# Kernel optimization log

Measured on AMD Instinct MI355X. Metric: run time of the kernel, lower is better.

The kernel has to match this reference:

```python
import jax, jax.numpy as jnp
import numpy as np

B, L, D_MODEL, H, D_K, D_V, C = 4, 2048, 512, 8, 64, 64, 5
LN_EPS = 1e-5


def setup_inputs() -> dict:
    key = jax.random.key(0)
    ks = jax.random.split(key, 9)
    u_k = min(int(C * np.log(L)), L)  # 38
    s = 1.0 / np.sqrt(D_MODEL)
    return {
        "input_Q": jax.random.normal(ks[0], (B, L, D_MODEL), jnp.float32),
        "input_K": jax.random.normal(ks[1], (B, L, D_MODEL), jnp.float32),
        "input_V": jax.random.normal(ks[2], (B, L, D_MODEL), jnp.float32),
        "W_Q": jax.random.normal(ks[3], (D_MODEL, H * D_K), jnp.float32) * s,
        "W_K": jax.random.normal(ks[4], (D_MODEL, H * D_K), jnp.float32) * s,
        "W_V": jax.random.normal(ks[5], (D_MODEL, H * D_V), jnp.float32) * s,
        "W_fc": jax.random.normal(ks[6], (H * D_V, D_MODEL), jnp.float32) * (1.0 / np.sqrt(H * D_V)),
        "ln_gamma": jnp.ones((D_MODEL,), jnp.float32),
        "ln_beta": jnp.zeros((D_MODEL,), jnp.float32),
        "index_sample": jax.random.randint(ks[7], (L, u_k), 0, L, jnp.int32),
    }


def reference(input_Q, input_K, input_V, W_Q, W_K, W_V, W_fc, ln_gamma, ln_beta, index_sample):
    Bb, L_Q, _ = input_Q.shape
    L_K = input_K.shape[1]
    u_q = min(int(C * np.log(L_Q)), L_Q)  # n_top queries kept

    # projections -> (B, H, L, d)
    Q = (input_Q @ W_Q).reshape(Bb, L_Q, H, D_K).transpose(0, 2, 1, 3)
    K = (input_K @ W_K).reshape(Bb, L_K, H, D_K).transpose(0, 2, 1, 3)
    V = (input_V @ W_V).reshape(Bb, L_K, H, D_V).transpose(0, 2, 1, 3)

    # sampled QK scores: gather u_k random keys per query position
    K_sample = K[:, :, index_sample, :]                      # (B,H,L_Q,u_k,d_k)
    QK_sample = jnp.einsum('bhqe,bhqke->bhqk', Q, K_sample)  # (B,H,L_Q,u_k)

    # sparsity measure M = max - mean, top-u_q queries
    M = QK_sample.max(axis=-1) - QK_sample.mean(axis=-1)     # (B,H,L_Q)
    _, idx = jax.lax.top_k(M, u_q)                           # (B,H,u_q)

    # attention only for selected queries
    Q_sel = jnp.take_along_axis(Q, idx[..., None], axis=2)   # (B,H,u_q,d_k)
    scores = jnp.einsum('bhue,bhke->bhuk', Q_sel, K) / np.sqrt(D_K)
    attn = jax.nn.softmax(scores, axis=-1)
    values = jnp.einsum('bhuk,bhkd->bhud', attn, V)          # (B,H,u_q,d_v)

    # initial context = mean of V (attn_mask is None), scatter selected rows
    context = jnp.broadcast_to(V.mean(axis=2, keepdims=True), (Bb, H, L_Q, D_V))
    bb = jnp.arange(Bb)[:, None, None]
    hh = jnp.arange(H)[None, :, None]
    context = context.at[bb, hh, idx].set(values)

    context = context.transpose(0, 2, 1, 3).reshape(Bb, L_Q, H * D_V)
    out = context @ W_fc                                     # dropout p=0.0

    y = out + input_Q
    mu = y.mean(axis=-1, keepdims=True)
    var = jnp.mean(jnp.square(y - mu), axis=-1, keepdims=True)
    y = (y - mu) / jnp.sqrt(var + LN_EPS) * ln_gamma + ln_beta
    return y, idx
```

## Files before the change

kernel.cpp:

```cpp
#include <hip/hip_runtime.h>
#include <hip/hip_bf16.h>

#define NB 4
#define NL 2048
#define NH 8
#define NDM 512
#define ND 64
#define KSPLIT 16
#define KTILE 32
#define QB 8

typedef __attribute__((ext_vector_type(8))) short short8b;
typedef __attribute__((ext_vector_type(4))) float f32x4;

__global__ void wconv(const float* __restrict__ W, unsigned short* __restrict__ WT) {
  const int g = blockIdx.x * 256 + threadIdx.x;
  const int k = g >> 9, c = g & 511;
  __hip_bfloat16 hb = __float2bfloat16(W[(size_t)k * 512 + c]);
  WT[(size_t)c * 512 + k] = *reinterpret_cast<unsigned short*>(&hb);
}

__global__ void vmean_colmean(const float* __restrict__ inV, float* __restrict__ parts) {
  const int b = blockIdx.x, seg = blockIdx.y, t = threadIdx.x;
  const float* p = inV + ((size_t)b * NL + seg * 32) * NDM;
  float s0 = 0.f, s1 = 0.f;
  for (int r = 0; r < 32; ++r) {
    s0 += p[(size_t)r * NDM + t];
    s1 += p[(size_t)r * NDM + 256 + t];
  }
  parts[((size_t)b * 64 + seg) * NDM + t] = s0;
  parts[((size_t)b * 64 + seg) * NDM + 256 + t] = s1;
}
__global__ void vmean_gemm(const float* __restrict__ parts, const float* __restrict__ Wv,
                           float* __restrict__ Vm) {
  __shared__ float cm[512];
  const int b = blockIdx.x, t = threadIdx.x;
  float a0 = 0.f, a1 = 0.f;
  for (int g = 0; g < 64; ++g) {
    a0 += parts[((size_t)b * 64 + g) * NDM + t];
    a1 += parts[((size_t)b * 64 + g) * NDM + 256 + t];
  }
  cm[t] = a0 * (1.f / 2048.f);
  cm[t + 256] = a1 * (1.f / 2048.f);
  __syncthreads();
  const int c0 = blockIdx.y * 256 + t;
  float acc = 0.f;
  for (int k = 0; k < 512; ++k) acc += cm[k] * Wv[(size_t)k * NDM + c0];
  Vm[b * 512 + c0] = acc;
}

__global__ __launch_bounds__(256, 4) void proj3(
    const float* __restrict__ AQ, const float* __restrict__ AK,
    const float* __restrict__ wQm, const float* __restrict__ wKm,
    int gh0, float* __restrict__ Qc, float* __restrict__ Kc) {
  __shared__ float As_[32 * 132];
  __shared__ float Ws_[32 * 68];
  const int tid = threadIdx.x;
  const int bm = blockIdx.x;
  const int hl = blockIdx.y;
  const int mat = blockIdx.z;
  const int bh = gh0 + hl;
  const int b = bh >> 3, h = bh & 7;
  const float* A = (mat == 0) ? AQ : AK;
  const float* W = (mat == 0) ? wQm : wKm;
  float* D = (mat == 0) ? Qc : Kc;
  const float* Ab = A + (size_t)b * NL * NDM;
  const int colbase = h * 64;
  const int tm = tid >> 4, tn = tid & 15;
  float acc[8][4] = {};
  for (int k0 = 0; k0 < 512; k0 += 32) {
#pragma unroll
    for (int i = 0; i < 4; ++i) {
      int s = tid + i * 256;
      int r = s >> 3, c4 = (s & 7) * 4;
      float4 v = *reinterpret_cast<const float4*>(Ab + (size_t)(bm * 128 + r) * 512 + k0 + c4);
      As_[(c4 + 0) * 132 + r] = v.x;
      As_[(c4 + 1) * 132 + r] = v.y;
      As_[(c4 + 2) * 132 + r] = v.z;
      As_[(c4 + 3) * 132 + r] = v.w;
    }
#pragma unroll
    for (int i = 0; i < 2; ++i) {
      int s = tid + i * 256;
      int r = s >> 4, c4 = (s & 15) * 4;
      *reinterpret_cast<float4*>(&Ws_[r * 68 + c4]) =
          *reinterpret_cast<const float4*>(W + (size_t)(k0 + r) * 512 + colbase + c4);
    }
    __syncthreads();
#pragma unroll
    for (int kk = 0; kk < 32; ++kk) {
      float4 a0 = *reinterpret_cast<const float4*>(&As_[kk * 132 + tm * 4]);
      float4 a1 = *reinterpret_cast<const float4*>(&As_[kk * 132 + 64 + tm * 4]);
      float4 w  = *reinterpret_cast<const float4*>(&Ws_[kk * 68 + tn * 4]);
      float a[8] = {a0.x, a0.y, a0.z, a0.w, a1.x, a1.y, a1.z, a1.w};
      float wv[4] = {w.x, w.y, w.z, w.w};
#pragma unroll
      for (int ii = 0; ii < 8; ++ii)
#pragma unroll
        for (int jj = 0; jj < 4; ++jj) acc[ii][jj] += a[ii] * wv[jj];
    }
    __syncthreads();
  }
#pragma unroll
  for (int ii = 0; ii < 8; ++ii) {
    int row = bm * 128 + ((ii < 4) ? (tm * 4 + ii) : (64 + tm * 4 + (ii - 4)));
    float4 v = make_float4(acc[ii][0], acc[ii][1], acc[ii][2], acc[ii][3]);
    *reinterpret_cast<float4*>(D + ((size_t)hl * NL + row) * ND + tn * 4) = v;
  }
}

__global__ __launch_bounds__(256) void projV_mfma(
    const float* __restrict__ AV, const unsigned short* __restrict__ WT,
    int gh0, float* __restrict__ Vc) {
  const int wv = threadIdx.x >> 6, l = threadIdx.x & 63;
  const int bm = blockIdx.x;
  const int hl = blockIdx.y;
  const int bh = gh0 + hl;
  const int b = bh >> 3, h = bh & 7;
  const float* Ab = AV + (size_t)b * NL * NDM;
  const int row = bm * 64 + wv * 16 + (l & 15);
  const int kg = (l >> 4) * 8;
  f32x4 acc0 = {}, acc1 = {}, acc2 = {}, acc3 = {};
  for (int k0 = 0; k0 < 512; k0 += 32) {
    const float* ap = Ab + (size_t)row * 512 + k0 + kg;
    float4 v0 = *reinterpret_cast<const float4*>(ap);
    float4 v1 = *reinterpret_cast<const float4*>(ap + 4);
    short8b af;
    {
      __hip_bfloat16 hb;
      hb = __float2bfloat16(v0.x); af[0] = *reinterpret_cast<short*>(&hb);
      hb = __float2bfloat16(v0.y); af[1] = *reinterpret_cast<short*>(&hb);
      hb = __float2bfloat16(v0.z); af[2] = *reinterpret_cast<short*>(&hb);
      hb = __float2bfloat16(v0.w); af[3] = *reinterpret_cast<short*>(&hb);
      hb = __float2bfloat16(v1.x); af[4] = *reinterpret_cast<short*>(&hb);
      hb = __float2bfloat16(v1.y); af[5] = *reinterpret_cast<short*>(&hb);
      hb = __float2bfloat16(v1.z); af[6] = *reinterpret_cast<short*>(&hb);
      hb = __float2bfloat16(v1.w); af[7] = *reinterpret_cast<short*>(&hb);
    }
    const unsigned short* wp = WT + (size_t)(h * 64 + (l & 15)) * 512 + k0 + kg;
    short8b b0 = *reinterpret_cast<const short8b*>(wp);
    short8b b1 = *reinterpret_cast<const short8b*>(wp + 16 * 512);
    short8b b2 = *reinterpret_cast<const short8b*>(wp + 32 * 512);
    short8b b3 = *reinterpret_cast<const short8b*>(wp + 48 * 512);
    acc0 = __builtin_amdgcn_mfma_f32_16x16x32_bf16(af, b0, acc0, 0, 0, 0);
    acc1 = __builtin_amdgcn_mfma_f32_16x16x32_bf16(af, b1, acc1, 0, 0, 0);
    acc2 = __builtin_amdgcn_mfma_f32_16x16x32_bf16(af, b2, acc2, 0, 0, 0);
    acc3 = __builtin_amdgcn_mfma_f32_16x16x32_bf16(af, b3, acc3, 0, 0, 0);
  }
  const int rbase = bm * 64 + wv * 16 + (l >> 4) * 4;
  const int col = l & 15;
#pragma unroll
  for (int j = 0; j < 4; ++j) {
    size_t o = ((size_t)hl * NL + rbase + j) * ND + col;
    Vc[o] = acc0[j];
    Vc[o + 16] = acc1[j];
    Vc[o + 32] = acc2[j];
    Vc[o + 48] = acc3[j];
  }
}

template <int UK>
__global__ __launch_bounds__(256) void sampleV_fused(
    const float* __restrict__ Q, const float* __restrict__ K,
    const int* __restrict__ sampP, float* __restrict__ M,
    const float* __restrict__ AV, const unsigned short* __restrict__ WT,
    int gh0, float* __restrict__ Vc, int nsampBlk) {
  if ((int)blockIdx.x >= nsampBlk) {
    const int vblk = blockIdx.x - nsampBlk;
    const int bm = vblk & 31;
    const int hl = vblk >> 5;
    const int wv = threadIdx.x >> 6, l = threadIdx.x & 63;
    const int bh = gh0 + hl;
    const int b = bh >> 3, h = bh & 7;
    const float* Ab = AV + (size_t)b * NL * NDM;
    const int row = bm * 64 + wv * 16 + (l & 15);
    const int kg = (l >> 4) * 8;
    f32x4 acc0 = {}, acc1 = {}, acc2 = {}, acc3 = {};
    for (int k0 = 0; k0 < 512; k0 += 32) {
      const float* ap = Ab + (size_t)row * 512 + k0 + kg;
      float4 v0 = *reinterpret_cast<const float4*>(ap);
      float4 v1 = *reinterpret_cast<const float4*>(ap + 4);
      short8b af;
      {
        __hip_bfloat16 hb;
        hb = __float2bfloat16(v0.x); af[0] = *reinterpret_cast<short*>(&hb);
        hb = __float2bfloat16(v0.y); af[1] = *reinterpret_cast<short*>(&hb);
        hb = __float2bfloat16(v0.z); af[2] = *reinterpret_cast<short*>(&hb);
        hb = __float2bfloat16(v0.w); af[3] = *reinterpret_cast<short*>(&hb);
        hb = __float2bfloat16(v1.x); af[4] = *reinterpret_cast<short*>(&hb);
        hb = __float2bfloat16(v1.y); af[5] = *reinterpret_cast<short*>(&hb);
        hb = __float2bfloat16(v1.z); af[6] = *reinterpret_cast<short*>(&hb);
        hb = __float2bfloat16(v1.w); af[7] = *reinterpret_cast<short*>(&hb);
      }
      const unsigned short* wp = WT + (size_t)(h * 64 + (l & 15)) * 512 + k0 + kg;
      short8b b0 = *reinterpret_cast<const short8b*>(wp);
      short8b b1 = *reinterpret_cast<const short8b*>(wp + 16 * 512);
      short8b b2 = *reinterpret_cast<const short8b*>(wp + 32 * 512);
      short8b b3 = *reinterpret_cast<const short8b*>(wp + 48 * 512);
      acc0 = __builtin_amdgcn_mfma_f32_16x16x32_bf16(af, b0, acc0, 0, 0, 0);
      acc1 = __builtin_amdgcn_mfma_f32_16x16x32_bf16(af, b1, acc1, 0, 0, 0);
      acc2 = __builtin_amdgcn_mfma_f32_16x16x32_bf16(af, b2, acc2, 0, 0, 0);
      acc3 = __builtin_amdgcn_mfma_f32_16x16x32_bf16(af, b3, acc3, 0, 0, 0);
    }
    const int rbase = bm * 64 + wv * 16 + (l >> 4) * 4;
    const int col = l & 15;
#pragma unroll
    for (int j = 0; j < 4; ++j) {
      size_t o = ((size_t)hl * NL + rbase + j) * ND + col;
      Vc[o] = acc0[j];
      Vc[o + 16] = acc1[j];
      Vc[o + 32] = acc2[j];
      Vc[o + 48] = acc3[j];
    }
    return;
  }
  __shared__ float KsAll[4][UK * 66];
  __shared__ float QsAll[4][68];
  const int wv = threadIdx.x >> 6, l = threadIdx.x & 63;
  const int gq = blockIdx.x * 4 + wv;
  const int hl = gq >> 11;
  const int q = gq & 2047;
  float* Ks = KsAll[wv];
  float* Qs = QsAll[wv];
  const float* Kb = K + (size_t)hl * NL * ND;
  Qs[l] = Q[(size_t)gq * ND + l];
  const int base = __builtin_amdgcn_readfirstlane(q) * UK;
#pragma unroll
  for (int r = 0; r < UK; ++r) {
    int kk = sampP[base + r] & (NL - 1);
    Ks[r * 66 + l] = Kb[(size_t)kk * ND + l];
  }
  __syncthreads();
  const int myk = (l < UK) ? l : (UK - 1);
  float acc = 0.f;
#pragma unroll
  for (int j = 0; j < 32; ++j) {
    float2 kv = *reinterpret_cast<const float2*>(&Ks[myk * 66 + 2 * j]);
    float2 qv = *reinterpret_cast<const float2*>(&Qs[2 * j]);
    acc += kv.x * qv.x + kv.y * qv.y;
  }
  float mval = (l < UK) ? acc : -1e30f;
  float sval = (l < UK) ? acc : 0.f;
#pragma unroll
  for (int o = 32; o; o >>= 1) {
    mval = fmaxf(mval, __shfl_xor(mval, o, 64));
    sval += __shfl_xor(sval, o, 64);
  }
  if (l == 0) M[gq] = mval - sval * (1.f / (float)UK);
}

__global__ void sample_scores_gen(const float* __restrict__ Q, const float* __restrict__ K,
                                  const int* __restrict__ sampP, float* __restrict__ M, int uk) {
  const int wave = threadIdx.x >> 6, lane = threadIdx.x & 63;
  const int gq = blockIdx.x * 4 + wave;
  const int hl = gq >> 11;
  const int q = gq & 2047;
  const float qv = Q[(size_t)gq * ND + lane];
  const float* Kbase = K + (size_t)hl * NL * ND;
  float mx = -1e30f, sm = 0.f;
  for (int k = 0; k < uk; ++k) {
    int kidx = sampP[q * uk + k] & (NL - 1);
    float p = qv * Kbase[(size_t)kidx * ND + lane];
#pragma unroll
    for (int o = 32; o; o >>= 1) p += __shfl_xor(p, o, 64);
    mx = fmaxf(mx, p);
    sm += p;
  }
  if (lane == 0) M[gq] = mx - sm / (float)uk;
}

__global__ void topk_kernel(const float* __restrict__ M, int* __restrict__ idxo,
                            float* __restrict__ outIdx, short* __restrict__ selmap,
                            int gh0, int uq) {
  __shared__ float mv[2048];
  __shared__ float bwv[4];
  __shared__ int bwi[4];
  const int bh = blockIdx.x, t = threadIdx.x;
  const int bhg = gh0 + bh;
  const int bb = bhg >> 3, hh = bhg & 7;
  float lv = -1e38f; int li = 1 << 30;
#pragma unroll
  for (int i = 0; i < 8; ++i) {
    int id = t + i * 256;
    float v = M[(size_t)bh * 2048 + id];
    mv[id] = v;
    if (v > lv || (v == lv && id < li)) { lv = v; li = id; }
  }
  __syncthreads();
  for (int it = 0; it < uq; ++it) {
    float bv = lv; int bi = li;
#pragma unroll
    for (int o = 32; o; o >>= 1) {
      float ov = __shfl_xor(bv, o, 64);
      int oi = __shfl_xor(bi, o, 64);
      if (ov > bv || (ov == bv && oi < bi)) { bv = ov; bi = oi; }
    }
    if ((t & 63) == 0) { bwv[t >> 6] = bv; bwi[t >> 6] = bi; }
    __syncthreads();
    float gb = bwv[0]; int gi = bwi[0];
#pragma unroll
    for (int w = 1; w < 4; ++w) {
      if (bwv[w] > gb || (bwv[w] == gb && bwi[w] < gi)) { gb = bwv[w]; gi = bwi[w]; }
    }
    const int sel = gi & (NL - 1);
    if (t == 0) {
      idxo[bh * uq + it] = sel;
      outIdx[bh * uq + it] = (float)sel;
      selmap[((size_t)bb * NL + sel) * NH + hh] = (short)it;
    }
    if ((sel & 255) == t) {
      mv[sel] = -1e38f;
      lv = -1e38f; li = 1 << 30;
#pragma unroll
      for (int i = 0; i < 8; ++i) {
        int id = t + i * 256;
        float v = mv[id];
        if (v > lv || (v == lv && id < li)) { lv = v; li = id; }
      }
    }
    __syncthreads();
  }
}

__global__ __launch_bounds__(256) void attn_part(
    const float* __restrict__ Qw, const float* __restrict__ Kw, const float* __restrict__ Vw,
    const int* __restrict__ idxo, float* __restrict__ pacc, float* __restrict__ pml, int uq) {
  __shared__ float Qs[QB][68];
  __shared__ float Ks[KTILE][68];
  __shared__ float Vs[KTILE][68];
  __shared__ float sc[QB][34];
  const int hl = blockIdx.x, qg = blockIdx.y, ks = blockIdx.z;
  const int t = threadIdx.x;
#pragma unroll
  for (int i = 0; i < 2; ++i) {
    int s = t + i * 256;
    int q = s >> 6, d = s & 63;
    int u = qg * QB + q;
    float v = 0.f;
    if (u < uq) {
      int qi = idxo[hl * uq + u] & (NL - 1);
      v = Qw[((size_t)hl * NL + qi) * ND + d];
    }
    Qs[q][d] = v;
  }
  float m_run = -1e30f, l_run = 0.f;
  float a0 = 0.f, a1 = 0.f;
  const int q2 = t >> 5, ln = t & 31;
  __syncthreads();
  const int kbeg = ks * (NL / KSPLIT);
  for (int k0 = kbeg; k0 < kbeg + NL / KSPLIT; k0 += KTILE) {
#pragma unroll
    for (int i = 0; i < 2; ++i) {
      int s = t + i * 256;
      int r = s >> 4, c4 = (s & 15) * 4;
      *reinterpret_cast<float4*>(&Ks[r][c4]) =
          *reinterpret_cast<const float4*>(Kw + ((size_t)hl * NL + k0 + r) * ND + c4);
      *reinterpret_cast<float4*>(&Vs[r][c4]) =
          *reinterpret_cast<const float4*>(Vw + ((size_t)hl * NL + k0 + r) * ND + c4);
    }
    __syncthreads();
    {
      const int q = t & 7, kk = t >> 3;
      float d0 = 0.f;
#pragma unroll
      for (int dd = 0; dd < 64; dd += 4) {
        float4 qv = *reinterpret_cast<const float4*>(&Qs[q][dd]);
        float4 ka = *reinterpret_cast<const float4*>(&Ks[kk][dd]);
        d0 += qv.x * ka.x + qv.y * ka.y + qv.z * ka.z + qv.w * ka.w;
      }
      sc[q][kk] = d0 * 0.125f;
    }
    __syncthreads();
    {
      float s0 = sc[q2][ln];
      float tmax = s0;
#pragma unroll
      for (int o = 16; o; o >>= 1) tmax = fmaxf(tmax, __shfl_xor(tmax, o, 64));
      float mnew = fmaxf(m_run, tmax);
      float scl = __expf(m_run - mnew);
      float p0 = __expf(s0 - mnew);
      float tsum = p0;
#pragma unroll
      for (int o = 16; o; o >>= 1) tsum += __shfl_xor(tsum, o, 64);
      l_run = l_run * scl + tsum;
      m_run = mnew;
      sc[q2][ln] = p0;
      a0 *= scl; a1 *= scl;
#pragma unroll 8
      for (int k = 0; k < KTILE; ++k) {
        float p = sc[q2][k];
        a0 += p * Vs[k][2 * ln];
        a1 += p * Vs[k][2 * ln + 1];
      }
    }
    __syncthreads();
  }
  const int u = qg * QB + q2;
  if (u < uq) {
    size_t g = ((size_t)hl * uq + u) * KSPLIT + ks;
    pacc[g * ND + 2 * ln] = a0;
    pacc[g * ND + 2 * ln + 1] = a1;
    if (ln == 0) { pml[g * 2] = m_run; pml[g * 2 + 1] = l_run; }
  }
}

__global__ void corr_merge(const float* __restrict__ pacc, const float* __restrict__ pml,
                           const float* __restrict__ Vm, const float* __restrict__ Wfc,
                           float* __restrict__ corr, int uq) {
  __shared__ float diff[64];
  const int g = blockIdx.x, t = threadIdx.x;
  const int bh = g / uq;
  const int h = bh & 7;
  if (t < 64) {
    float mstar = -1e30f;
#pragma unroll
    for (int s = 0; s < KSPLIT; ++s) mstar = fmaxf(mstar, pml[((size_t)g * KSPLIT + s) * 2]);
    float num = 0.f, den = 0.f;
#pragma unroll
    for (int s = 0; s < KSPLIT; ++s) {
      float e = __expf(pml[((size_t)g * KSPLIT + s) * 2] - mstar);
      den += e * pml[((size_t)g * KSPLIT + s) * 2 + 1];
      num += e * pacc[((size_t)g * KSPLIT + s) * ND + t];
    }
    diff[t] = num / den - Vm[(size_t)bh * 64 + t];
  }
  __syncthreads();
  float a0 = 0.f, a1 = 0.f;
#pragma unroll
  for (int d = 0; d < 64; ++d) {
    a0 += diff[d] * Wfc[(size_t)(h * 64 + d) * 512 + t];
    a1 += diff[d] * Wfc[(size_t)(h * 64 + d) * 512 + t + 256];
  }
  corr[(size_t)g * 512 + t] = a0;
  corr[(size_t)g * 512 + t + 256] = a1;
}

__global__ void base_gemm(const float* __restrict__ Vm, const float* __restrict__ Wfc,
                          float* __restrict__ base) {
  __shared__ float vm[512];
  const int b = blockIdx.x, t = threadIdx.x;
  vm[t] = Vm[b * 512 + t];
  vm[t + 256] = Vm[b * 512 + t + 256];
  __syncthreads();
  const int c0 = blockIdx.y * 256 + t;
  float acc = 0.f;
  for (int k = 0; k < 512; ++k) acc += vm[k] * Wfc[(size_t)k * 512 + c0];
  base[b * 512 + c0] = acc;
}

__global__ void ln_fused(const float* __restrict__ base, const float* __restrict__ resid,
                         const float* __restrict__ corr, const short* __restrict__ selmap,
                         const float* __restrict__ gamma, const float* __restrict__ beta,
                         float* __restrict__ out, int uq) {
  __shared__ float red[256];
  const int row = blockIdx.x, t = threadIdx.x;
  const int b = row >> 11;
  float y0 = base[b * 512 + t] + resid[(size_t)row * 512 + t];
  float y1 = base[b * 512 + 256 + t] + resid[(size_t)row * 512 + 256 + t];
#pragma unroll
  for (int h = 0; h < NH; ++h) {
    int s = selmap[(size_t)row * NH + h];
    if (s >= 0 && s < uq) {
      const float* cp = corr + (size_t)((b * NH + h) * uq + s) * 512;
      y0 += cp[t];
      y1 += cp[t + 256];
    }
  }
  red[t] = y0 + y1;
  __syncthreads();
  for (int s = 128; s; s >>= 1) { if (t < s) red[t] += red[t + s]; __syncthreads(); }
  const float mu = red[0] * (1.f / 512.f);
  __syncthreads();
  const float d0 = y0 - mu, d1 = y1 - mu;
  red[t] = d0 * d0 + d1 * d1;
  __syncthreads();
  for (int s = 128; s; s >>= 1) { if (t < s) red[t] += red[t + s]; __syncthreads(); }
  const float rs = rsqrtf(red[0] * (1.f / 512.f) + 1e-5f);
  __syncthreads();
  out[(size_t)row * 512 + t] = d0 * rs * gamma[t] + beta[t];
  out[(size_t)row * 512 + 256 + t] = d1 * rs * gamma[256 + t] + beta[256 + t];
}

extern "C" void kernel_launch(void* const* d_in, const int* in_sizes, int n_in,
                              void* d_out, int out_size, void* d_ws, size_t ws_size,
                              hipStream_t stream) {
  const float* inQ = (const float*)d_in[0];
  const float* inK = (const float*)d_in[1];
  const float* inV = (const float*)d_in[2];
  const float* wQ = (const float*)d_in[3];
  const float* wK = (const float*)d_in[4];
  const float* wV = (const float*)d_in[5];
  const float* wFC = (const float*)d_in[6];
  const float* gamma = (const float*)d_in[7];
  const float* beta = (const float*)d_in[8];
  const int* samp = (const int*)d_in[9];

  const int nsamp = in_sizes[9];
  const int uk = nsamp / NL;
  const int uq = uk;
  const int nqg = (uq + QB - 1) / QB;

  if (out_size < NB * NL * NDM + NB * NH * uq) return;

  const size_t perH = 3 * 131072 + 2048;
  const size_t fixed = (size_t)32 * uq * KSPLIT * 64 + (size_t)32 * uq * KSPLIT * 2
                     + 2048 + 2048 + (size_t)32 * uq * 512 + (size_t)32 * uq
                     + 32768 + 131072 + 131072 + 256;
  int hcg = 0;
  for (int c = 32; c >= 1; c >>= 1) {
    if ((perH * (size_t)c + fixed + 256) * 4ull <= ws_size) { hcg = c; break; }
  }
  if (hcg == 0) return;

  float* ws = (float*)d_ws;
  float* Qc = ws;
  float* Kc = Qc + (size_t)hcg * 131072;
  float* Vc = Kc + (size_t)hcg * 131072;
  float* Mb = Vc + (size_t)hcg * 131072;
  float* pacc = Mb + (size_t)hcg * 2048;
  float* pml = pacc + (size_t)32 * uq * KSPLIT * 64;
  float* Vm = pml + (size_t)32 * uq * KSPLIT * 2;
  float* base = Vm + 2048;
  float* corr = base + 2048;
  int* idxo = (int*)(corr + (size_t)32 * uq * 512);
  short* selmap = (short*)(idxo + (size_t)32 * uq);
  unsigned short* WTv = (unsigned short*)(selmap + 65536);
  float* vparts = (float*)(WTv + 262144);

  float* out = (float*)d_out;
  float* outIdx = out + (size_t)NB * NL * NDM;

  wconv<<<1024, 256, 0, stream>>>(wV, WTv);
  vmean_colmean<<<dim3(NB, 64), 256, 0, stream>>>(inV, vparts);
  vmean_gemm<<<dim3(NB, 2), 256, 0, stream>>>(vparts, wV, Vm);
  hipMemsetAsync(selmap, 0xFF, (size_t)NB * NL * NH * sizeof(short), stream);

  for (int gh0 = 0; gh0 < NB * NH; gh0 += hcg) {
    proj3<<<dim3(16, hcg, 2), 256, 0, stream>>>(inQ, inK, wQ, wK, gh0, Qc, Kc);
    if (uk == 38) {
      const int nsampBlk = hcg * NL / 4;
      sampleV_fused<38><<<nsampBlk + hcg * 32, 256, 0, stream>>>(
          Qc, Kc, samp, Mb, inV, WTv, gh0, Vc, nsampBlk);
    } else {
      projV_mfma<<<dim3(32, hcg), 256, 0, stream>>>(inV, WTv, gh0, Vc);
      sample_scores_gen<<<hcg * NL / 4, 256, 0, stream>>>(Qc, Kc, samp, Mb, uk);
    }
    topk_kernel<<<hcg, 256, 0, stream>>>(Mb, idxo + (size_t)gh0 * uq,
                                         outIdx + (size_t)gh0 * uq, selmap, gh0, uq);
    attn_part<<<dim3(hcg, nqg, KSPLIT), 256, 0, stream>>>(
        Qc, Kc, Vc, idxo + (size_t)gh0 * uq,
        pacc + (size_t)gh0 * uq * KSPLIT * 64,
        pml + (size_t)gh0 * uq * KSPLIT * 2, uq);
  }

  base_gemm<<<dim3(NB, 2), 256, 0, stream>>>(Vm, wFC, base);
  corr_merge<<<NB * NH * uq, 256, 0, stream>>>(pacc, pml, Vm, wFC, corr, uq);
  ln_fused<<<NB * NL, 256, 0, stream>>>(base, inQ, corr, selmap, gamma, beta, out, uq);
}
```

Measured before the change: 365.5 us.

## Compute Q/K projections with split-bf16 MFMA emulating fp32 precision

```diff
diff --git a/kernel.cpp b/kernel.cpp
--- a/kernel.cpp
+++ b/kernel.cpp
@@ -13,11 +13,33 @@
 typedef __attribute__((ext_vector_type(8))) short short8b;
 typedef __attribute__((ext_vector_type(4))) float f32x4;
 
-__global__ void wconv(const float* __restrict__ W, unsigned short* __restrict__ WT) {
+static __device__ __forceinline__ unsigned short bfbits(float v) {
+  __hip_bfloat16 h = __float2bfloat16(v);
+  return *reinterpret_cast<unsigned short*>(&h);
+}
+static __device__ __forceinline__ float bf2f(unsigned short u) {
+  union { unsigned int i; float f; } c; c.i = ((unsigned int)u) << 16; return c.f;
+}
+
+__global__ void wconv3(const float* __restrict__ wQ, const float* __restrict__ wK,
+                       const float* __restrict__ wV,
+                       unsigned short* __restrict__ WTq3, unsigned short* __restrict__ WTk3,
+                       unsigned short* __restrict__ WTv) {
   const int g = blockIdx.x * 256 + threadIdx.x;
+  const int m = blockIdx.y;
   const int k = g >> 9, c = g & 511;
-  __hip_bfloat16 hb = __float2bfloat16(W[(size_t)k * 512 + c]);
-  WT[(size_t)c * 512 + k] = *reinterpret_cast<unsigned short*>(&hb);
+  const float* W = (m == 0) ? wQ : (m == 1) ? wK : wV;
+  const float v = W[(size_t)k * 512 + c];
+  const unsigned short h1 = bfbits(v);
+  if (m == 2) { WTv[(size_t)c * 512 + k] = h1; return; }
+  const float r1 = v - bf2f(h1);
+  const unsigned short h2 = bfbits(r1);
+  const float r2 = r1 - bf2f(h2);
+  const unsigned short h3 = bfbits(r2);
+  unsigned short* WT = (m == 0) ? WTq3 : WTk3;
+  WT[(size_t)c * 512 + k] = h1;
+  WT[262144 + (size_t)c * 512 + k] = h2;
+  WT[524288 + (size_t)c * 512 + k] = h3;
 }
 
 __global__ void vmean_colmean(const float* __restrict__ inV, float* __restrict__ parts) {
@@ -49,64 +71,61 @@
   Vm[b * 512 + c0] = acc;
 }
 
-__global__ __launch_bounds__(256, 4) void proj3(
+__global__ __launch_bounds__(256) void projQK_mfma(
     const float* __restrict__ AQ, const float* __restrict__ AK,
-    const float* __restrict__ wQm, const float* __restrict__ wKm,
+    const unsigned short* __restrict__ WTq3, const unsigned short* __restrict__ WTk3,
     int gh0, float* __restrict__ Qc, float* __restrict__ Kc) {
-  __shared__ float As_[32 * 132];
-  __shared__ float Ws_[32 * 68];
-  const int tid = threadIdx.x;
+  const int wv = threadIdx.x >> 6, l = threadIdx.x & 63;
   const int bm = blockIdx.x;
   const int hl = blockIdx.y;
   const int mat = blockIdx.z;
   const int bh = gh0 + hl;
   const int b = bh >> 3, h = bh & 7;
-  const float* A = (mat == 0) ? AQ : AK;
-  const float* W = (mat == 0) ? wQm : wKm;
+  const float* Ab = ((mat == 0) ? AQ : AK) + (size_t)b * NL * NDM;
+  const unsigned short* WT3 = (mat == 0) ? WTq3 : WTk3;
   float* D = (mat == 0) ? Qc : Kc;
-  const float* Ab = A + (size_t)b * NL * NDM;
-  const int colbase = h * 64;
-  const int tm = tid >> 4, tn = tid & 15;
-  float acc[8][4] = {};
+  const int row = bm * 64 + wv * 16 + (l & 15);
+  const int kg = (l >> 4) * 8;
+  f32x4 acc[4] = {};
   for (int k0 = 0; k0 < 512; k0 += 32) {
-#pragma unroll
-    for (int i = 0; i < 4; ++i) {
-      int s = tid + i * 256;
-      int r = s >> 3, c4 = (s & 7) * 4;
-      float4 v = *reinterpret_cast<const float4*>(Ab + (size_t)(bm * 128 + r) * 512 + k0 + c4);
-      As_[(c4 + 0) * 132 + r] = v.x;
-      As_[(c4 + 1) * 132 + r] = v.y;
-      As_[(c4 + 2) * 132 + r] = v.z;
-      As_[(c4 + 3) * 132 + r] = v.w;
-    }
-#pragma unroll
-    for (int i = 0; i < 2; ++i) {
-      int s = tid + i * 256;
-      int r = s >> 4, c4 = (s & 15) * 4;
-      *reinterpret_cast<float4*>(&Ws_[r * 68 + c4]) =
-          *reinterpret_cast<const float4*>(W + (size_t)(k0 + r) * 512 + colbase + c4);
-    }
-    __syncthreads();
-#pragma unroll
-    for (int kk = 0; kk < 32; ++kk) {
-      float4 a0 = *reinterpret_cast<const float4*>(&As_[kk * 132 + tm * 4]);
-      float4 a1 = *reinterpret_cast<const float4*>(&As_[kk * 132 + 64 + tm * 4]);
-      float4 w  = *reinterpret_cast<const float4*>(&Ws_[kk * 68 + tn * 4]);
-      float a[8] = {a0.x, a0.y, a0.z, a0.w, a1.x, a1.y, a1.z, a1.w};
-      float wv[4] = {w.x, w.y, w.z, w.w};
-#pragma unroll
-      for (int ii = 0; ii < 8; ++ii)
-#pragma unroll
-        for (int jj = 0; jj < 4; ++jj) acc[ii][jj] += a[ii] * wv[jj];
-    }
-    __syncthreads();
-  }
-#pragma unroll
-  for (int ii = 0; ii < 8; ++ii) {
-    int row = bm * 128 + ((ii < 4) ? (tm * 4 + ii) : (64 + tm * 4 + (ii - 4)));
-    float4 v = make_float4(acc[ii][0], acc[ii][1], acc[ii][2], acc[ii][3]);
-    *reinterpret_cast<float4*>(D + ((size_t)hl * NL + row) * ND + tn * 4) = v;
-  }
+    const float* ap = Ab + (size_t)row * 512 + k0 + kg;
+    float4 v0 = *reinterpret_cast<const float4*>(ap);
+    float4 v1 = *reinterpret_cast<const float4*>(ap + 4);
+    float va[8] = {v0.x, v0.y, v0.z, v0.w, v1.x, v1.y, v1.z, v1.w};
+    short8b ah, am, al;
+#pragma unroll
+    for (int j = 0; j < 8; ++j) {
+      unsigned short h1 = bfbits(va[j]);
+      float r1 = va[j] - bf2f(h1);
+      unsigned short h2 = bfbits(r1);
+      float r2 = r1 - bf2f(h2);
+      unsigned short h3 = bfbits(r2);
+      ah[j] = (short)h1;
+      am[j] = (short)h2;
+      al[j] = (short)h3;
+    }
+    const unsigned short* wp = WT3 + (size_t)(h * 64 + (l & 15)) * 512 + k0 + kg;
+#pragma unroll
+    for (int cb = 0; cb < 4; ++cb) {
+      const unsigned short* w = wp + (size_t)cb * 16 * 512;
+      short8b bh_ = *reinterpret_cast<const short8b*>(w);
+      short8b bm_ = *reinterpret_cast<const short8b*>(w + 262144);
+      short8b bl_ = *reinterpret_cast<const short8b*>(w + 524288);
+      acc[cb] = __builtin_amdgcn_mfma_f32_16x16x32_bf16(ah, bh_, acc[cb], 0, 0, 0);
+      acc[cb] = __builtin_amdgcn_mfma_f32_16x16x32_bf16(ah, bm_, acc[cb], 0, 0, 0);
+      acc[cb] = __builtin_amdgcn_mfma_f32_16x16x32_bf16(am, bh_, acc[cb], 0, 0, 0);
+      acc[cb] = __builtin_amdgcn_mfma_f32_16x16x32_bf16(ah, bl_, acc[cb], 0, 0, 0);
+      acc[cb] = __builtin_amdgcn_mfma_f32_16x16x32_bf16(al, bh_, acc[cb], 0, 0, 0);
+      acc[cb] = __builtin_amdgcn_mfma_f32_16x16x32_bf16(am, bm_, acc[cb], 0, 0, 0);
+    }
+  }
+  const int rbase = bm * 64 + wv * 16 + (l >> 4) * 4;
+  const int col = l & 15;
+#pragma unroll
+  for (int cb = 0; cb < 4; ++cb)
+#pragma unroll
+    for (int j = 0; j < 4; ++j)
+      D[((size_t)hl * NL + rbase + j) * ND + cb * 16 + col] = acc[cb][j];
 }
 
 __global__ __launch_bounds__(256) void projV_mfma(
@@ -126,17 +145,10 @@
     float4 v0 = *reinterpret_cast<const float4*>(ap);
     float4 v1 = *reinterpret_cast<const float4*>(ap + 4);
     short8b af;
-    {
-      __hip_bfloat16 hb;
-      hb = __float2bfloat16(v0.x); af[0] = *reinterpret_cast<short*>(&hb);
-      hb = __float2bfloat16(v0.y); af[1] = *reinterpret_cast<short*>(&hb);
-      hb = __float2bfloat16(v0.z); af[2] = *reinterpret_cast<short*>(&hb);
-      hb = __float2bfloat16(v0.w); af[3] = *reinterpret_cast<short*>(&hb);
-      hb = __float2bfloat16(v1.x); af[4] = *reinterpret_cast<short*>(&hb);
-      hb = __float2bfloat16(v1.y); af[5] = *reinterpret_cast<short*>(&hb);
-      hb = __float2bfloat16(v1.z); af[6] = *reinterpret_cast<short*>(&hb);
-      hb = __float2bfloat16(v1.w); af[7] = *reinterpret_cast<short*>(&hb);
-    }
+    af[0] = (short)bfbits(v0.x); af[1] = (short)bfbits(v0.y);
+    af[2] = (short)bfbits(v0.z); af[3] = (short)bfbits(v0.w);
+    af[4] = (short)bfbits(v1.x); af[5] = (short)bfbits(v1.y);
+    af[6] = (short)bfbits(v1.z); af[7] = (short)bfbits(v1.w);
     const unsigned short* wp = WT + (size_t)(h * 64 + (l & 15)) * 512 + k0 + kg;
     short8b b0 = *reinterpret_cast<const short8b*>(wp);
     short8b b1 = *reinterpret_cast<const short8b*>(wp + 16 * 512);
@@ -181,17 +193,10 @@
       float4 v0 = *reinterpret_cast<const float4*>(ap);
       float4 v1 = *reinterpret_cast<const float4*>(ap + 4);
       short8b af;
-      {
-        __hip_bfloat16 hb;
-        hb = __float2bfloat16(v0.x); af[0] = *reinterpret_cast<short*>(&hb);
-        hb = __float2bfloat16(v0.y); af[1] = *reinterpret_cast<short*>(&hb);
-        hb = __float2bfloat16(v0.z); af[2] = *reinterpret_cast<short*>(&hb);
-        hb = __float2bfloat16(v0.w); af[3] = *reinterpret_cast<short*>(&hb);
-        hb = __float2bfloat16(v1.x); af[4] = *reinterpret_cast<short*>(&hb);
-        hb = __float2bfloat16(v1.y); af[5] = *reinterpret_cast<short*>(&hb);
-        hb = __float2bfloat16(v1.z); af[6] = *reinterpret_cast<short*>(&hb);
-        hb = __float2bfloat16(v1.w); af[7] = *reinterpret_cast<short*>(&hb);
-      }
+      af[0] = (short)bfbits(v0.x); af[1] = (short)bfbits(v0.y);
+      af[2] = (short)bfbits(v0.z); af[3] = (short)bfbits(v0.w);
+      af[4] = (short)bfbits(v1.x); af[5] = (short)bfbits(v1.y);
+      af[6] = (short)bfbits(v1.z); af[7] = (short)bfbits(v1.w);
       const unsigned short* wp = WT + (size_t)(h * 64 + (l & 15)) * 512 + k0 + kg;
       short8b b0 = *reinterpret_cast<const short8b*>(wp);
       short8b b1 = *reinterpret_cast<const short8b*>(wp + 16 * 512);
@@ -505,7 +510,7 @@
   const size_t perH = 3 * 131072 + 2048;
   const size_t fixed = (size_t)32 * uq * KSPLIT * 64 + (size_t)32 * uq * KSPLIT * 2
                      + 2048 + 2048 + (size_t)32 * uq * 512 + (size_t)32 * uq
-                     + 32768 + 131072 + 131072 + 256;
+                     + 32768 + 131072 + 393216 + 393216 + 131072 + 256;
   int hcg = 0;
   for (int c = 32; c >= 1; c >>= 1) {
     if ((perH * (size_t)c + fixed + 256) * 4ull <= ws_size) { hcg = c; break; }
@@ -525,18 +530,20 @@
   int* idxo = (int*)(corr + (size_t)32 * uq * 512);
   short* selmap = (short*)(idxo + (size_t)32 * uq);
   unsigned short* WTv = (unsigned short*)(selmap + 65536);
-  float* vparts = (float*)(WTv + 262144);
+  unsigned short* WTq3 = WTv + 262144;
+  unsigned short* WTk3 = WTq3 + 786432;
+  float* vparts = (float*)(WTk3 + 786432);
 
   float* out = (float*)d_out;
   float* outIdx = out + (size_t)NB * NL * NDM;
 
-  wconv<<<1024, 256, 0, stream>>>(wV, WTv);
+  wconv3<<<dim3(1024, 3), 256, 0, stream>>>(wQ, wK, wV, WTq3, WTk3, WTv);
   vmean_colmean<<<dim3(NB, 64), 256, 0, stream>>>(inV, vparts);
   vmean_gemm<<<dim3(NB, 2), 256, 0, stream>>>(vparts, wV, Vm);
   hipMemsetAsync(selmap, 0xFF, (size_t)NB * NL * NH * sizeof(short), stream);
 
   for (int gh0 = 0; gh0 < NB * NH; gh0 += hcg) {
-    proj3<<<dim3(16, hcg, 2), 256, 0, stream>>>(inQ, inK, wQ, wK, gh0, Qc, Kc);
+    projQK_mfma<<<dim3(32, hcg, 2), 256, 0, stream>>>(inQ, inK, WTq3, WTk3, gh0, Qc, Kc);
     if (uk == 38) {
       const int nsampBlk = hcg * NL / 4;
       sampleV_fused<38><<<nsampBlk + hcg * 32, 256, 0, stream>>>(
```

After: 461.4 us. +26.2%, slower.
